# Kernel optimization log

Measured on AMD Instinct MI355X. Metric: run time of the kernel, lower is better.

Reference implementation:

```python
import jax, jax.numpy as jnp
import numpy as np

NUM_KNNS = 200
TEMPERATURE = 0.07
NUM_CLASSES = 1000


def setup_inputs() -> dict:
    key = jax.random.key(0)
    k1, k2, k3, k4 = jax.random.split(key, 4)
    N, D, K = 1024, 512, 65536
    # features and queue are L2-normalized (queue init is normal_l2)
    features = jax.random.normal(k1, (N, D), jnp.float32)
    features = features / jnp.linalg.norm(features, axis=-1, keepdims=True)
    queue_features = jax.random.normal(k2, (K, D), jnp.float32)
    queue_features = queue_features / jnp.linalg.norm(queue_features, axis=-1, keepdims=True)
    labels = jax.random.randint(k3, (N,), 0, NUM_CLASSES, dtype=jnp.int32)
    queue_labels = jax.random.randint(k4, (K,), 0, NUM_CLASSES, dtype=jnp.int32)
    return {
        "features": features,
        "queue_features": queue_features,
        "labels": labels,
        "queue_labels": queue_labels,
        "queue_ptr": 0,
    }


def reference(features, queue_features, labels, queue_labels, queue_ptr):
    # --- kNN accuracy ---
    # similarity matmul: [N, K]
    sim = jnp.einsum('nd,kd->nk', features, queue_features)
    sim_weight, sim_indices = jax.lax.top_k(sim, k=NUM_KNNS)  # [N, k]
    sim_weight = jnp.exp(sim_weight / TEMPERATURE)
    # gather neighbor labels (equivalent to the one-hot einsum in the original)
    sim_labels = queue_labels[sim_indices]  # [N, k] int32
    one_hot_labels = jax.nn.one_hot(sim_labels, NUM_CLASSES, dtype=sim_weight.dtype)  # [N, k, C]
    pred_scores = jnp.sum(one_hot_labels * sim_weight[..., None], axis=1)  # [N, C]
    pred_labels = jnp.argmax(pred_scores, axis=-1)
    accuracy = jnp.mean((pred_labels == labels).astype(jnp.float32))

    # --- circular queue scatter update ---
    N = features.shape[0]
    K = queue_features.shape[0]
    inds = jnp.arange(N) + queue_ptr
    new_queue_features = queue_features.at[inds].set(features)
    new_queue_labels = queue_labels.at[inds].set(labels)
    new_queue_ptr = (queue_ptr + N) % K
    return accuracy, new_queue_features, new_queue_labels, new_queue_ptr
```

## Files before the change

### kernel.cpp

```cpp
#include <hip/hip_runtime.h>
#include <math.h>

#define N_ROWS 1024
#define DIM    512
#define KQ     65536
#define KNN    200
#define NCLS   1000
#define NBINS  4096
#define CAP    2048
#define INV_T  14.285714285714286f

typedef unsigned short u16;
typedef __attribute__((ext_vector_type(8))) short short8;
typedef __attribute__((ext_vector_type(4))) float f32x4;
struct alignas(8) U16x4 { u16 x, y, z, w; };

#define GLOAD_LDS16(g, l)                                               \
    __builtin_amdgcn_global_load_lds(                                   \
        (__attribute__((address_space(1))) void*)(g),                   \
        (__attribute__((address_space(3))) void*)(l), 16, 0, 0)

__device__ __forceinline__ void split1(float x, u16& h, u16& l) {
    unsigned u = __float_as_uint(x);
    unsigned hr = (u + 0x7FFFu + ((u >> 16) & 1u)) >> 16;
    float hf = __uint_as_float(hr << 16);
    float lo = x - hf;
    unsigned ul = __float_as_uint(lo);
    unsigned lr = (ul + 0x7FFFu + ((ul >> 16) & 1u)) >> 16;
    h = (u16)hr; l = (u16)lr;
}

#define QF_BLOCKS (KQ * DIM / 4 / 256)
#define FT_BLOCKS (N_ROWS * DIM / 4 / 256)

__global__ __launch_bounds__(256) void fused_update_split_kernel(
    const float* __restrict__ feats, const float* __restrict__ qf,
    const int* __restrict__ labels, const int* __restrict__ ql,
    const int* __restrict__ qptr,
    float* __restrict__ out_qf, float* __restrict__ out_ql,
    float* __restrict__ out_ptr,
    u16* __restrict__ Bhi, u16* __restrict__ Blo,
    u16* __restrict__ Ahi, u16* __restrict__ Alo) {
    int ptr = qptr[0];
    int b = blockIdx.x;
    if (b < QF_BLOCKS) {
        size_t t = (size_t)b * 256 + threadIdx.x;
        size_t idx = t * 4;
        int row = (int)(idx >> 9);
        int col = (int)(idx & 511);
        float4 v = *(const float4*)(qf + idx);
        U16x4 h, l;
        split1(v.x, h.x, l.x); split1(v.y, h.y, l.y);
        split1(v.z, h.z, l.z); split1(v.w, h.w, l.w);
        *(U16x4*)(Bhi + idx) = h;
        *(U16x4*)(Blo + idx) = l;
        int d = row - ptr; if (d < 0) d += KQ;
        float4 o = (d < N_ROWS) ? *(const float4*)(feats + (size_t)d * DIM + col) : v;
        *(float4*)(out_qf + idx) = o;
        if (col == 0)
            out_ql[row] = (float)((d < N_ROWS) ? labels[d] : ql[row]);
    } else {
        size_t t = (size_t)(b - QF_BLOCKS) * 256 + threadIdx.x;
        size_t idx = t * 4;
        float4 v = *(const float4*)(feats + idx);
        U16x4 h, l;
        split1(v.x, h.x, l.x); split1(v.y, h.y, l.y);
        split1(v.z, h.z, l.z); split1(v.w, h.w, l.w);
        *(U16x4*)(Ahi + idx) = h;
        *(U16x4*)(Alo + idx) = l;
        if (t == 0) out_ptr[0] = (float)((ptr + N_ROWS) % KQ);
    }
}

#define NKT 24

#define STAGE8(kt_, dA, dB)                                                    \
  {                                                                            \
    const u16* Ap_ = ((kt_) < 16) ? Ahi : Alo;                                 \
    const u16* Bp_ = (((kt_) >> 3) == 1) ? Blo : Bhi;                          \
    int ke_ = ((kt_) & 7) << 6;                                                \
    const u16* ga_ = Ap_ + (size_t)(r0A + srow) * DIM + ke_ + scol;            \
    const u16* gb_ = Bp_ + (size_t)(r0B + srow) * DIM + ke_ + scol;            \
    GLOAD_LDS16(ga_ + (size_t)(8 * w0) * DIM,         &dA[0][w0 * 512]);       \
    GLOAD_LDS16(ga_ + (size_t)(8 * w1) * DIM,         &dA[0][w1 * 512]);       \
    GLOAD_LDS16(ga_ + (size_t)(128 + 8 * w0) * DIM,   &dA[1][w0 * 512]);       \
    GLOAD_LDS16(ga_ + (size_t)(128 + 8 * w1) * DIM,   &dA[1][w1 * 512]);       \
    GLOAD_LDS16(gb_ + (size_t)(8 * w0) * DIM,         &dB[0][w0 * 512]);       \
    GLOAD_LDS16(gb_ + (size_t)(8 * w1) * DIM,         &dB[0][w1 * 512]);       \
    GLOAD_LDS16(gb_ + (size_t)(128 + 8 * w0) * DIM,   &dB[1][w0 * 512]);       \
    GLOAD_LDS16(gb_ + (size_t)(128 + 8 * w1) * DIM,   &dB[1][w1 * 512]);       \
  }

#define MM(t_, u_)                                                             \
  acc[t_][u_] = __builtin_amdgcn_mfma_f32_16x16x32_bf16(                       \
      fa[(t_) & 3][0], fb[u_][0], acc[t_][u_], 0, 0, 0);                       \
  acc[t_][u_] = __builtin_amdgcn_mfma_f32_16x16x32_bf16(                       \
      fa[(t_) & 3][1], fb[u_][1], acc[t_][u_], 0, 0, 0);

#define TILE(kt_, RA, RB, SA, SB, DO_STAGE)                                    \
  {                                                                            \
    asm volatile("s_waitcnt vmcnt(0)" ::: "memory");                           \
    __builtin_amdgcn_s_barrier();                                              \
    const u16* aH_ = &RA[wm][0];                                               \
    const u16* bH_ = &RB[wn >> 1][bB];                                         \
                                                                  \
    _Pragma("unroll") for (int t = 0; t < 4; ++t) {                            \
      fa[t][0] = *(const short8*)(aH_ + t * 1024 + aoff + c0);                 \
      fa[t][1] = *(const short8*)(aH_ + t * 1024 + aoff + c1);                 \
    }                                                                          \
    _Pragma("unroll") for (int u = 0; u < 2; ++u) {                            \
      fb[u][0] = *(const short8*)(bH_ + u * 1024 + aoff + c0);                 \
      fb[u][1] = *(const short8*)(bH_ + u * 1024 + aoff + c1);                 \
    }                                                                          \
    if (DO_STAGE) STAGE8((kt_) + 1, SA, SB);                                   \
    __builtin_amdgcn_s_barrier();                                              \
    __builtin_amdgcn_s_setprio(1);                                             \
    _Pragma("unroll") for (int t = 0; t < 4; ++t) {                            \
      MM(t, 0); MM(t, 1);                                                      \
    }                                                                          \
    __builtin_amdgcn_s_setprio(0);                                             \
    __builtin_amdgcn_s_barrier();                                              \
                                                                  \
    _Pragma("unroll") for (int u = 2; u < 4; ++u) {                            \
      fb[u][0] = *(const short8*)(bH_ + u * 1024 + aoff + c0);                 \
      fb[u][1] = *(const short8*)(bH_ + u * 1024 + aoff + c1);                 \
    }                                                                          \
    __builtin_amdgcn_s_barrier();                                              \
    __builtin_amdgcn_s_setprio(1);                                             \
    _Pragma("unroll") for (int t = 0; t < 4; ++t) {                            \
      MM(t, 2); MM(t, 3);                                                      \
    }                                                                          \
    __builtin_amdgcn_s_setprio(0);                                             \
    __builtin_amdgcn_s_barrier();                                              \
                                                                  \
    _Pragma("unroll") for (int t = 0; t < 4; ++t) {                            \
      fa[t][0] = *(const short8*)(aH_ + (t + 4) * 1024 + aoff + c0);           \
      fa[t][1] = *(const short8*)(aH_ + (t + 4) * 1024 + aoff + c1);           \
    }                                                                          \
    __builtin_amdgcn_s_barrier();                                              \
    __builtin_amdgcn_s_setprio(1);                                             \
    _Pragma("unroll") for (int t = 4; t < 8; ++t) {                            \
      MM(t, 2); MM(t, 3);                                                      \
    }                                                                          \
    __builtin_amdgcn_s_setprio(0);                                             \
    __builtin_amdgcn_s_barrier();                                              \
                                                                  \
    __builtin_amdgcn_s_setprio(1);                                             \
    _Pragma("unroll") for (int t = 4; t < 8; ++t) {                            \
      MM(t, 0); MM(t, 1);                                                      \
    }                                                                          \
    __builtin_amdgcn_s_setprio(0);                                             \
  }

__global__ __launch_bounds__(512, 2) void gemm256_kernel(
    const u16* __restrict__ Ahi, const u16* __restrict__ Alo,
    const u16* __restrict__ Bhi, const u16* __restrict__ Blo,
    float* __restrict__ C) {
    __shared__ u16 sA0[2][8192], sB0[2][8192];
    __shared__ u16 sA1[2][8192], sB1[2][8192];

    int tid = threadIdx.x;
    int wv = tid >> 6, lane = tid & 63;
    int r = lane & 15, q = lane >> 4;
    int wm = wv >> 2, wn = wv & 3;
    int srow = lane >> 3;
    int scol = ((lane & 7) ^ (lane >> 3)) << 3;
    int w0 = wv, w1 = wv + 8;
    int aoff = r << 6;
    int c0 = (q << 3) ^ ((r & 7) << 3);
    int c1 = (32 | (q << 3)) ^ ((r & 7) << 3);
    int bB = (wn & 1) << 12;
    int r0A = blockIdx.y << 8;
    int r0B = blockIdx.x << 8;

    f32x4 acc[8][4] = {};
    short8 fa[4][2], fb[4][2];

    STAGE8(0, sA0, sB0);

    for (int kt = 0; kt < NKT; kt += 2) {
        TILE(kt,     sA0, sB0, sA1, sB1, 1);
        TILE(kt + 1, sA1, sB1, sA0, sB0, (kt + 2) < NKT);
    }

#pragma unroll
    for (int t = 0; t < 8; ++t)
#pragma unroll
        for (int u = 0; u < 4; ++u)
#pragma unroll
            for (int g = 0; g < 4; ++g) {
                int row = r0A + wm * 128 + t * 16 + q * 4 + g;
                int col = r0B + wn * 64 + u * 16 + r;
                C[(size_t)row * KQ + col] = acc[t][u][g];
            }
}

__global__ __launch_bounds__(256, 4) void gemm_mfma_kernel(
    const u16* __restrict__ Ahi, const u16* __restrict__ Alo,
    const u16* __restrict__ Bhi, const u16* __restrict__ Blo,
    float* __restrict__ C) {
    __shared__ u16 sA[2][128 * 32];
    __shared__ u16 sB[2][128 * 32];

    int tid = threadIdx.x;
    int wave = tid >> 6, lane = tid & 63;
    int q = lane >> 4, r = lane & 15;
    int bn = blockIdx.x, bm = blockIdx.y;
    int wm = wave & 1, wn = wave >> 1;

    const u16* gplane = (wave == 0) ? Ahi : (wave == 1) ? Alo
                      : (wave == 2) ? Bhi : Blo;
    int prow0 = (wave < 2) ? bm * 128 : bn * 128;
    const u16* gbase = gplane + (size_t)prow0 * DIM;
    u16* lbase = (wave == 0) ? sA[0] : (wave == 1) ? sA[1]
               : (wave == 2) ? sB[0] : sB[1];
    int lrow = lane >> 2;
    int lchunk = lane & 3;

    f32x4 acc[4][4] = {};

    for (int kt = 0; kt < DIM; kt += 32) {
        __syncthreads();
#pragma unroll
        for (int s = 0; s < 8; ++s) {
            const u16* g = gbase + (size_t)(s * 16 + lrow) * DIM + kt + lchunk * 8;
            GLOAD_LDS16(g, lbase + s * 512);
        }
        __syncthreads();

        short8 fa[2][4], fb[2][4];
#pragma unroll
        for (int t = 0; t < 4; ++t) {
            int am = wm * 64 + t * 16 + r;
            fa[0][t] = *(const short8*)&sA[0][am * 32 + q * 8];
            fa[1][t] = *(const short8*)&sA[1][am * 32 + q * 8];
            int bn_ = wn * 64 + t * 16 + r;
            fb[0][t] = *(const short8*)&sB[0][bn_ * 32 + q * 8];
            fb[1][t] = *(const short8*)&sB[1][bn_ * 32 + q * 8];
        }
#pragma unroll
        for (int i = 0; i < 4; ++i)
#pragma unroll
            for (int j = 0; j < 4; ++j) {
                acc[i][j] = __builtin_amdgcn_mfma_f32_16x16x32_bf16(
                    fa[0][i], fb[0][j], acc[i][j], 0, 0, 0);
                acc[i][j] = __builtin_amdgcn_mfma_f32_16x16x32_bf16(
                    fa[0][i], fb[1][j], acc[i][j], 0, 0, 0);
                acc[i][j] = __builtin_amdgcn_mfma_f32_16x16x32_bf16(
                    fa[1][i], fb[0][j], acc[i][j], 0, 0, 0);
            }
    }

#pragma unroll
    for (int i = 0; i < 4; ++i)
#pragma unroll
        for (int j = 0; j < 4; ++j)
#pragma unroll
            for (int g = 0; g < 4; ++g) {
                int row = bm * 128 + wm * 64 + i * 16 + q * 4 + g;
                int col = bn * 128 + wn * 64 + j * 16 + r;
                C[(size_t)row * KQ + col] = acc[i][j][g];
            }
}

#define LSTR 68
#define LA(k, m) ((k) * LSTR + (m))

__global__ __launch_bounds__(256) void gemm_nt_kernel(
    const float* __restrict__ A, const float* __restrict__ B,
    float* __restrict__ C) {
    __shared__ float As[32 * LSTR];
    __shared__ float Bs[32 * LSTR];
    int tid = threadIdx.x;
    int bn = blockIdx.x, bm = blockIdx.y;
    int tx = tid & 15, ty = tid >> 4;
    int lm = tid >> 3;
    int lk = (tid & 7) * 4;
    const float* Ab = A + (size_t)bm * 64 * DIM;
    const float* Bb = B + (size_t)bn * 64 * DIM;
    float acc[4][4] = {};
    for (int kt = 0; kt < DIM; kt += 32) {
        float4 a0 = *(const float4*)(Ab + (size_t)lm * DIM + kt + lk);
        float4 a1 = *(const float4*)(Ab + (size_t)(lm + 32) * DIM + kt + lk);
        float4 b0 = *(const float4*)(Bb + (size_t)lm * DIM + kt + lk);
        float4 b1 = *(const float4*)(Bb + (size_t)(lm + 32) * DIM + kt + lk);
        __syncthreads();
        As[LA(lk + 0, lm)] = a0.x;  As[LA(lk + 1, lm)] = a0.y;
        As[LA(lk + 2, lm)] = a0.z;  As[LA(lk + 3, lm)] = a0.w;
        As[LA(lk + 0, lm + 32)] = a1.x;  As[LA(lk + 1, lm + 32)] = a1.y;
        As[LA(lk + 2, lm + 32)] = a1.z;  As[LA(lk + 3, lm + 32)] = a1.w;
        Bs[LA(lk + 0, lm)] = b0.x;  Bs[LA(lk + 1, lm)] = b0.y;
        Bs[LA(lk + 2, lm)] = b0.z;  Bs[LA(lk + 3, lm)] = b0.w;
        Bs[LA(lk + 0, lm + 32)] = b1.x;  Bs[LA(lk + 1, lm + 32)] = b1.y;
        Bs[LA(lk + 2, lm + 32)] = b1.z;  Bs[LA(lk + 3, lm + 32)] = b1.w;
        __syncthreads();
#pragma unroll
        for (int kk = 0; kk < 32; ++kk) {
            float4 av = *(const float4*)&As[LA(kk, ty * 4)];
            float4 bv = *(const float4*)&Bs[LA(kk, tx * 4)];
            float a_[4] = {av.x, av.y, av.z, av.w};
            float b_[4] = {bv.x, bv.y, bv.z, bv.w};
#pragma unroll
            for (int i = 0; i < 4; ++i)
#pragma unroll
                for (int j = 0; j < 4; ++j) acc[i][j] += a_[i] * b_[j];
        }
    }
    for (int i = 0; i < 4; ++i) {
        float4 o = make_float4(acc[i][0], acc[i][1], acc[i][2], acc[i][3]);
        *(float4*)(C + (size_t)(bm * 64 + ty * 4 + i) * KQ + bn * 64 + tx * 4) = o;
    }
}

__device__ __forceinline__ unsigned order_key(float v) {
    unsigned u = __float_as_uint(v);
    return u ^ ((u & 0x80000000u) ? 0xFFFFFFFFu : 0x80000000u);
}

__global__ __launch_bounds__(1024) void topk_kernel(
    const float* __restrict__ sim, int r0,
    const int* __restrict__ ql, const int* __restrict__ labels,
    float* __restrict__ flags) {
    __shared__ unsigned hist[NBINS];
    __shared__ float cval[CAP];
    __shared__ int   cidx[CAP];
    __shared__ float scores[NCLS];
    __shared__ unsigned wsum[16];
    __shared__ float rb[16];
    __shared__ int   rc[16];
    __shared__ int s_bstar, s_ncand;

    int row = blockIdx.x;
    int tid = threadIdx.x;
    int lane = tid & 63;
    int wv = tid >> 6;
    const float4* s4 = (const float4*)(sim + (size_t)row * KQ);

    hist[tid] = 0; hist[tid + 1024] = 0; hist[tid + 2048] = 0; hist[tid + 3072] = 0;
    if (tid == 0) s_ncand = 0;
    __syncthreads();

    for (int i4 = tid; i4 < KQ / 4; i4 += 1024) {
        float4 v = s4[i4];
        atomicAdd(&hist[order_key(v.x) >> 20], 1u);
        atomicAdd(&hist[order_key(v.y) >> 20], 1u);
        atomicAdd(&hist[order_key(v.z) >> 20], 1u);
        atomicAdd(&hist[order_key(v.w) >> 20], 1u);
    }
    __syncthreads();

    unsigned loc = hist[4 * tid] + hist[4 * tid + 1] +
                   hist[4 * tid + 2] + hist[4 * tid + 3];
    unsigned x = loc;
#pragma unroll
    for (int off = 1; off < 64; off <<= 1) {
        unsigned y = __shfl_down(x, off);
        if (lane + off < 64) x += y;
    }
    if (lane == 0) wsum[wv] = x;
    __syncthreads();
    unsigned above = 0;
#pragma unroll
    for (int w2 = 0; w2 < 16; ++w2)
        if (w2 > wv) above += wsum[w2];
    unsigned running = above + x - loc;
    for (int j = 3; j >= 0; --j) {
        unsigned c = hist[4 * tid + j];
        if (running < KNN && running + c >= KNN) s_bstar = 4 * tid + j;
        running += c;
    }
    __syncthreads();
    int bstar = s_bstar;

    for (int i4 = tid; i4 < KQ / 4; i4 += 1024) {
        float4 v = s4[i4];
        float vv[4] = {v.x, v.y, v.z, v.w};
#pragma unroll
        for (int c = 0; c < 4; ++c) {
            if ((int)(order_key(vv[c]) >> 20) >= bstar) {
                int p = atomicAdd(&s_ncand, 1);
                if (p < CAP) { cval[p] = vv[c]; cidx[p] = i4 * 4 + c; }
            }
        }
    }
    if (tid < NCLS) scores[tid] = 0.f;
    __syncthreads();

    int M = s_ncand; if (M > CAP) M = CAP;
    for (int c = tid; c < M; c += 1024) {
        float v = cval[c]; int id = cidx[c];
        int rank = 0;
        for (int j = 0; j < M; ++j) {
            float vj = cval[j];
            if (vj > v || (vj == v && cidx[j] < id)) rank++;
        }
        if (rank < KNN) {
            float w = expf(v * INV_T);
            atomicAdd(&scores[ql[id]], w);
        }
    }
    __syncthreads();

    float b2 = (tid < NCLS) ? scores[tid] : -1.f;
    int   c2 = (tid < NCLS) ? tid : 0x3FFFFFFF;
#pragma unroll
    for (int off = 1; off < 64; off <<= 1) {
        float ob = __shfl_down(b2, off);
        int   oc = __shfl_down(c2, off);
        if (lane + off < 64 && (ob > b2 || (ob == b2 && oc < c2))) { b2 = ob; c2 = oc; }
    }
    if (lane == 0) { rb[wv] = b2; rc[wv] = c2; }
    __syncthreads();
    if (tid < 64) {
        float b3 = -1.f; int c3 = 0x3FFFFFFF;
        if (tid < 16) { b3 = rb[tid]; c3 = rc[tid]; }
#pragma unroll
        for (int off = 1; off < 16; off <<= 1) {
            float ob = __shfl_down(b3, off);
            int   oc = __shfl_down(c3, off);
            if (tid + off < 16 && (ob > b3 || (ob == b3 && oc < c3))) { b3 = ob; c3 = oc; }
        }
        if (tid == 0)
            flags[r0 + row] = (c3 == labels[r0 + row]) ? 1.0f : 0.0f;
    }
}

__global__ __launch_bounds__(256) void acc_kernel(
    const float* __restrict__ flags, float* __restrict__ out) {
    __shared__ float r[256];
    int tid = threadIdx.x;
    r[tid] = flags[tid] + flags[tid + 256] + flags[tid + 512] + flags[tid + 768];
    __syncthreads();
    for (int off = 128; off; off >>= 1) {
        if (tid < off) r[tid] += r[tid + off];
        __syncthreads();
    }
    if (tid == 0) out[0] = r[0] * (1.0f / 1024.0f);
}

extern "C" void kernel_launch(void* const* d_in, const int* in_sizes, int n_in,
                              void* d_out, int out_size, void* d_ws, size_t ws_size,
                              hipStream_t stream) {
    const float* feats  = (const float*)d_in[0];
    const float* qf     = (const float*)d_in[1];
    const int*   labels = (const int*)d_in[2];
    const int*   ql     = (const int*)d_in[3];
    const int*   qptr   = (const int*)d_in[4];

    float* out     = (float*)d_out;
    float* out_qf  = out + 1;
    float* out_ql  = out_qf + (size_t)KQ * DIM;
    float* out_ptr = out_ql + KQ;

    const size_t bplane = (size_t)KQ * DIM;
    const size_t aplane = (size_t)N_ROWS * DIM;

    int CH = 0;
    for (int c = 512; c >= 128; c >>= 1) {
        size_t need = 2 * bplane * 2 + 2 * aplane * 2 +
                      (size_t)c * KQ * 4 + N_ROWS * 4;
        if (need <= ws_size) { CH = c; break; }
    }

    if (CH > 0) {
        u16* Bhi = (u16*)d_ws;
        u16* Blo = Bhi + bplane;
        u16* Ahi = Blo + bplane;
        u16* Alo = Ahi + aplane;
        float* sim   = (float*)(Alo + aplane);
        float* flags = sim + (size_t)CH * KQ;

        fused_update_split_kernel<<<QF_BLOCKS + FT_BLOCKS, 256, 0, stream>>>(
            feats, qf, labels, ql, qptr, out_qf, out_ql, out_ptr,
            Bhi, Blo, Ahi, Alo);

        int nchunks = N_ROWS / CH;
        for (int c = 0; c < nchunks; ++c) {
            if (CH >= 256) {
                dim3 g(KQ / 256, CH / 256);
                gemm256_kernel<<<g, 512, 0, stream>>>(
                    Ahi + (size_t)c * CH * DIM, Alo + (size_t)c * CH * DIM,
                    Bhi, Blo, sim);
            } else {
                dim3 g(KQ / 128, CH / 128);
                gemm_mfma_kernel<<<g, 256, 0, stream>>>(
                    Ahi + (size_t)c * CH * DIM, Alo + (size_t)c * CH * DIM,
                    Bhi, Blo, sim);
            }
            topk_kernel<<<CH, 1024, 0, stream>>>(sim, c * CH, ql, labels, flags);
        }
        acc_kernel<<<1, 256, 0, stream>>>(flags, out);
    } else {
        int CHf = 256;
        while (CHf > 64 &&
               ((size_t)CHf * KQ * sizeof(float) + N_ROWS * sizeof(float)) > ws_size)
            CHf >>= 1;
        float* sim   = (float*)d_ws;
        float* flags = (float*)((char*)d_ws + (size_t)CHf * KQ * sizeof(float));
        fused_update_split_kernel<<<QF_BLOCKS + FT_BLOCKS, 256, 0, stream>>>(
            feats, qf, labels, ql, qptr, out_qf, out_ql, out_ptr,
            (u16*)sim, (u16*)sim, (u16*)sim, (u16*)sim);
        int nchunks = N_ROWS / CHf;
        for (int c = 0; c < nchunks; ++c) {
            const float* A = feats + (size_t)c * CHf * DIM;
            dim3 g(KQ / 64, CHf / 64);
            gemm_nt_kernel<<<g, 256, 0, stream>>>(A, qf, sim);
            topk_kernel<<<CHf, 1024, 0, stream>>>(sim, c * CHf, ql, labels, flags);
        }
        acc_kernel<<<1, 256, 0, stream>>>(flags, out);
    }
}
```

Before: 579.6 us.

## Use per-wave-pair packed 16-bit histograms and 512-thread blocks in top-k

The top-k kernel now runs with 512 threads per block and builds four privatized histograms, one per pair of waves. Each histogram has 2048 bins packed as two 16-bit counters per 32-bit word. This is meant to reduce LDS atomic contention during histogramming and to shrink the block for better occupancy. The coarser bins (shift by 21 instead of 20) can admit more candidates past the threshold, which raises the O(M^2) rank cost and the risk of overflowing CAP.

```diff
diff --git a/kernel.cpp b/kernel.cpp
--- a/kernel.cpp
+++ b/kernel.cpp
@@ -6,7 +6,6 @@
 #define KQ     65536
 #define KNN    200
 #define NCLS   1000
-#define NBINS  4096
 #define CAP    2048
 #define INV_T  14.285714285714286f
 
@@ -312,22 +311,25 @@
     }
 }
 
+#define NB2   2048
+#define NW2   1024
+
 __device__ __forceinline__ unsigned order_key(float v) {
     unsigned u = __float_as_uint(v);
     return u ^ ((u & 0x80000000u) ? 0xFFFFFFFFu : 0x80000000u);
 }
 
-__global__ __launch_bounds__(1024) void topk_kernel(
+__global__ __launch_bounds__(512) void topk_kernel(
     const float* __restrict__ sim, int r0,
     const int* __restrict__ ql, const int* __restrict__ labels,
     float* __restrict__ flags) {
-    __shared__ unsigned hist[NBINS];
+    __shared__ unsigned wh[4][NW2];
     __shared__ float cval[CAP];
     __shared__ int   cidx[CAP];
     __shared__ float scores[NCLS];
-    __shared__ unsigned wsum[16];
-    __shared__ float rb[16];
-    __shared__ int   rc[16];
+    __shared__ unsigned wsum[8];
+    __shared__ float rb[8];
+    __shared__ int   rc[8];
     __shared__ int s_bstar, s_ncand;
 
     int row = blockIdx.x;
@@ -336,21 +338,33 @@
     int wv = tid >> 6;
     const float4* s4 = (const float4*)(sim + (size_t)row * KQ);
 
-    hist[tid] = 0; hist[tid + 1024] = 0; hist[tid + 2048] = 0; hist[tid + 3072] = 0;
+#pragma unroll
+    for (int i = 0; i < 8; ++i) ((unsigned*)wh)[tid + 512 * i] = 0;
     if (tid == 0) s_ncand = 0;
     __syncthreads();
 
-    for (int i4 = tid; i4 < KQ / 4; i4 += 1024) {
+    unsigned* myh = wh[wv >> 1];
+    for (int i4 = tid; i4 < KQ / 4; i4 += 512) {
         float4 v = s4[i4];
-        atomicAdd(&hist[order_key(v.x) >> 20], 1u);
-        atomicAdd(&hist[order_key(v.y) >> 20], 1u);
-        atomicAdd(&hist[order_key(v.z) >> 20], 1u);
-        atomicAdd(&hist[order_key(v.w) >> 20], 1u);
-    }
-    __syncthreads();
-
-    unsigned loc = hist[4 * tid] + hist[4 * tid + 1] +
-                   hist[4 * tid + 2] + hist[4 * tid + 3];
+        unsigned k0 = order_key(v.x) >> 21, k1 = order_key(v.y) >> 21;
+        unsigned k2 = order_key(v.z) >> 21, k3 = order_key(v.w) >> 21;
+        atomicAdd(&myh[k0 >> 1], 1u << ((k0 & 1) << 4));
+        atomicAdd(&myh[k1 >> 1], 1u << ((k1 & 1) << 4));
+        atomicAdd(&myh[k2 >> 1], 1u << ((k2 & 1) << 4));
+        atomicAdd(&myh[k3 >> 1], 1u << ((k3 & 1) << 4));
+    }
+    __syncthreads();
+
+    unsigned cnt0 = 0, cnt1 = 0, cnt2 = 0, cnt3 = 0;
+#pragma unroll
+    for (int c = 0; c < 4; ++c) {
+        unsigned a = wh[c][2 * tid];
+        unsigned b = wh[c][2 * tid + 1];
+        cnt0 += a & 0xFFFFu; cnt1 += a >> 16;
+        cnt2 += b & 0xFFFFu; cnt3 += b >> 16;
+    }
+    unsigned loc = cnt0 + cnt1 + cnt2 + cnt3;
+
     unsigned x = loc;
 #pragma unroll
     for (int off = 1; off < 64; off <<= 1) {
@@ -361,33 +375,36 @@
     __syncthreads();
     unsigned above = 0;
 #pragma unroll
-    for (int w2 = 0; w2 < 16; ++w2)
+    for (int w2 = 0; w2 < 8; ++w2)
         if (w2 > wv) above += wsum[w2];
     unsigned running = above + x - loc;
+    unsigned cnts[4] = {cnt0, cnt1, cnt2, cnt3};
+#pragma unroll
     for (int j = 3; j >= 0; --j) {
-        unsigned c = hist[4 * tid + j];
+        unsigned c = cnts[j];
         if (running < KNN && running + c >= KNN) s_bstar = 4 * tid + j;
         running += c;
     }
     __syncthreads();
     int bstar = s_bstar;
 
-    for (int i4 = tid; i4 < KQ / 4; i4 += 1024) {
+    for (int i4 = tid; i4 < KQ / 4; i4 += 512) {
         float4 v = s4[i4];
         float vv[4] = {v.x, v.y, v.z, v.w};
 #pragma unroll
         for (int c = 0; c < 4; ++c) {
-            if ((int)(order_key(vv[c]) >> 20) >= bstar) {
+            if ((int)(order_key(vv[c]) >> 21) >= bstar) {
                 int p = atomicAdd(&s_ncand, 1);
                 if (p < CAP) { cval[p] = vv[c]; cidx[p] = i4 * 4 + c; }
             }
         }
     }
-    if (tid < NCLS) scores[tid] = 0.f;
+    scores[tid] = 0.f;
+    if (tid + 512 < NCLS) scores[tid + 512] = 0.f;
     __syncthreads();
 
     int M = s_ncand; if (M > CAP) M = CAP;
-    for (int c = tid; c < M; c += 1024) {
+    for (int c = tid; c < M; c += 512) {
         float v = cval[c]; int id = cidx[c];
         int rank = 0;
         for (int j = 0; j < M; ++j) {
@@ -401,8 +418,10 @@
     }
     __syncthreads();
 
-    float b2 = (tid < NCLS) ? scores[tid] : -1.f;
-    int   c2 = (tid < NCLS) ? tid : 0x3FFFFFFF;
+    float sa = (tid < NCLS) ? scores[tid] : -1.f;
+    float sb = (tid + 512 < NCLS) ? scores[tid + 512] : -1.f;
+    float b2; int c2;
+    if (sb > sa) { b2 = sb; c2 = tid + 512; } else { b2 = sa; c2 = tid; }
 #pragma unroll
     for (int off = 1; off < 64; off <<= 1) {
         float ob = __shfl_down(b2, off);
@@ -413,12 +432,12 @@
     __syncthreads();
     if (tid < 64) {
         float b3 = -1.f; int c3 = 0x3FFFFFFF;
-        if (tid < 16) { b3 = rb[tid]; c3 = rc[tid]; }
-#pragma unroll
-        for (int off = 1; off < 16; off <<= 1) {
+        if (tid < 8) { b3 = rb[tid]; c3 = rc[tid]; }
+#pragma unroll
+        for (int off = 1; off < 8; off <<= 1) {
             float ob = __shfl_down(b3, off);
             int   oc = __shfl_down(c3, off);
-            if (tid + off < 16 && (ob > b3 || (ob == b3 && oc < c3))) { b3 = ob; c3 = oc; }
+            if (tid + off < 8 && (ob > b3 || (ob == b3 && oc < c3))) { b3 = ob; c3 = oc; }
         }
         if (tid == 0)
             flags[r0 + row] = (c3 == labels[r0 + row]) ? 1.0f : 0.0f;
@@ -487,7 +506,7 @@
                     Ahi + (size_t)c * CH * DIM, Alo + (size_t)c * CH * DIM,
                     Bhi, Blo, sim);
             }
-            topk_kernel<<<CH, 1024, 0, stream>>>(sim, c * CH, ql, labels, flags);
+            topk_kernel<<<CH, 512, 0, stream>>>(sim, c * CH, ql, labels, flags);
         }
         acc_kernel<<<1, 256, 0, stream>>>(flags, out);
     } else {
@@ -505,7 +524,7 @@
             const float* A = feats + (size_t)c * CHf * DIM;
             dim3 g(KQ / 64, CHf / 64);
             gemm_nt_kernel<<<g, 256, 0, stream>>>(A, qf, sim);
-            topk_kernel<<<CHf, 1024, 0, stream>>>(sim, c * CHf, ql, labels, flags);
+            topk_kernel<<<CHf, 512, 0, stream>>>(sim, c * CHf, ql, labels, flags);
         }
         acc_kernel<<<1, 256, 0, stream>>>(flags, out);
     }
```

New measurement: 629.1 us. 8.5% more time.

## Emit 16-bit order keys from GEMM epilogue and scan keys in top-k

Applied to the files above, without the earlier changes.

The GEMM epilogue now writes a 16-bit monotone order key for every similarity next to the fp32 value. The top-k kernel builds its histogram and selects candidates by reading these half-width keys, then gathers the full fp32 values only for the candidates. This is meant to halve the bytes read in the two full-row passes of top-k. In exchange the GEMM writes an extra 2 bytes per element with scattered 16-bit stores, and the workspace grows, which may shrink the chunk size.

```diff
diff --git a/kernel.cpp b/kernel.cpp
--- a/kernel.cpp
+++ b/kernel.cpp
@@ -19,6 +19,11 @@
     __builtin_amdgcn_global_load_lds(                                   \
         (__attribute__((address_space(1))) void*)(g),                   \
         (__attribute__((address_space(3))) void*)(l), 16, 0, 0)
+
+__device__ __forceinline__ unsigned order_key(float v) {
+    unsigned u = __float_as_uint(v);
+    return u ^ ((u & 0x80000000u) ? 0xFFFFFFFFu : 0x80000000u);
+}
 
 __device__ __forceinline__ void split1(float x, u16& h, u16& l) {
     unsigned u = __float_as_uint(x);
@@ -155,7 +160,7 @@
 __global__ __launch_bounds__(512, 2) void gemm256_kernel(
     const u16* __restrict__ Ahi, const u16* __restrict__ Alo,
     const u16* __restrict__ Bhi, const u16* __restrict__ Blo,
-    float* __restrict__ C) {
+    float* __restrict__ C, u16* __restrict__ Ck) {
     __shared__ u16 sA0[2][8192], sB0[2][8192];
     __shared__ u16 sA1[2][8192], sB1[2][8192];
 
@@ -191,14 +196,17 @@
             for (int g = 0; g < 4; ++g) {
                 int row = r0A + wm * 128 + t * 16 + q * 4 + g;
                 int col = r0B + wn * 64 + u * 16 + r;
-                C[(size_t)row * KQ + col] = acc[t][u][g];
+                float v = acc[t][u][g];
+                size_t off = (size_t)row * KQ + col;
+                C[off] = v;
+                Ck[off] = (u16)(order_key(v) >> 16);
             }
 }
 
 __global__ __launch_bounds__(256, 4) void gemm_mfma_kernel(
     const u16* __restrict__ Ahi, const u16* __restrict__ Alo,
     const u16* __restrict__ Bhi, const u16* __restrict__ Blo,
-    float* __restrict__ C) {
+    float* __restrict__ C, u16* __restrict__ Ck) {
     __shared__ u16 sA[2][128 * 32];
     __shared__ u16 sB[2][128 * 32];
 
@@ -259,7 +267,10 @@
             for (int g = 0; g < 4; ++g) {
                 int row = bm * 128 + wm * 64 + i * 16 + q * 4 + g;
                 int col = bn * 128 + wn * 64 + j * 16 + r;
-                C[(size_t)row * KQ + col] = acc[i][j][g];
+                float v = acc[i][j][g];
+                size_t off = (size_t)row * KQ + col;
+                C[off] = v;
+                Ck[off] = (u16)(order_key(v) >> 16);
             }
 }
 
@@ -312,13 +323,20 @@
     }
 }
 
-__device__ __forceinline__ unsigned order_key(float v) {
-    unsigned u = __float_as_uint(v);
-    return u ^ ((u & 0x80000000u) ? 0xFFFFFFFFu : 0x80000000u);
+__global__ __launch_bounds__(256) void keygen_kernel(
+    const float* __restrict__ sim, u16* __restrict__ keys) {
+    size_t i = ((size_t)blockIdx.x * 256 + threadIdx.x) * 4;
+    float4 v = *(const float4*)(sim + i);
+    U16x4 k;
+    k.x = (u16)(order_key(v.x) >> 16);
+    k.y = (u16)(order_key(v.y) >> 16);
+    k.z = (u16)(order_key(v.z) >> 16);
+    k.w = (u16)(order_key(v.w) >> 16);
+    *(U16x4*)(keys + i) = k;
 }
 
 __global__ __launch_bounds__(1024) void topk_kernel(
-    const float* __restrict__ sim, int r0,
+    const float* __restrict__ sim, const u16* __restrict__ keys, int r0,
     const int* __restrict__ ql, const int* __restrict__ labels,
     float* __restrict__ flags) {
     __shared__ unsigned hist[NBINS];
@@ -334,18 +352,23 @@
     int tid = threadIdx.x;
     int lane = tid & 63;
     int wv = tid >> 6;
-    const float4* s4 = (const float4*)(sim + (size_t)row * KQ);
+    const uint4* k8 = (const uint4*)(keys + (size_t)row * KQ);
+    const float* srow = sim + (size_t)row * KQ;
 
     hist[tid] = 0; hist[tid + 1024] = 0; hist[tid + 2048] = 0; hist[tid + 3072] = 0;
     if (tid == 0) s_ncand = 0;
     __syncthreads();
 
-    for (int i4 = tid; i4 < KQ / 4; i4 += 1024) {
-        float4 v = s4[i4];
-        atomicAdd(&hist[order_key(v.x) >> 20], 1u);
-        atomicAdd(&hist[order_key(v.y) >> 20], 1u);
-        atomicAdd(&hist[order_key(v.z) >> 20], 1u);
-        atomicAdd(&hist[order_key(v.w) >> 20], 1u);
+    for (int i8 = tid; i8 < KQ / 8; i8 += 1024) {
+        uint4 w = k8[i8];
+        atomicAdd(&hist[(w.x >> 4) & 0xFFFu], 1u);
+        atomicAdd(&hist[ w.x >> 20          ], 1u);
+        atomicAdd(&hist[(w.y >> 4) & 0xFFFu], 1u);
+        atomicAdd(&hist[ w.y >> 20          ], 1u);
+        atomicAdd(&hist[(w.z >> 4) & 0xFFFu], 1u);
+        atomicAdd(&hist[ w.z >> 20          ], 1u);
+        atomicAdd(&hist[(w.w >> 4) & 0xFFFu], 1u);
+        atomicAdd(&hist[ w.w >> 20          ], 1u);
     }
     __syncthreads();
 
@@ -372,21 +395,29 @@
     __syncthreads();
     int bstar = s_bstar;
 
-    for (int i4 = tid; i4 < KQ / 4; i4 += 1024) {
-        float4 v = s4[i4];
-        float vv[4] = {v.x, v.y, v.z, v.w};
-#pragma unroll
-        for (int c = 0; c < 4; ++c) {
-            if ((int)(order_key(vv[c]) >> 20) >= bstar) {
+    for (int i8 = tid; i8 < KQ / 8; i8 += 1024) {
+        uint4 w = k8[i8];
+        int base = i8 * 8;
+        unsigned words[4] = {w.x, w.y, w.z, w.w};
+#pragma unroll
+        for (int t = 0; t < 4; ++t) {
+            if ((int)((words[t] >> 4) & 0xFFFu) >= bstar) {
                 int p = atomicAdd(&s_ncand, 1);
-                if (p < CAP) { cval[p] = vv[c]; cidx[p] = i4 * 4 + c; }
+                if (p < CAP) cidx[p] = base + 2 * t;
             }
+            if ((int)(words[t] >> 20) >= bstar) {
+                int p = atomicAdd(&s_ncand, 1);
+                if (p < CAP) cidx[p] = base + 2 * t + 1;
+            }
         }
     }
     if (tid < NCLS) scores[tid] = 0.f;
     __syncthreads();
 
     int M = s_ncand; if (M > CAP) M = CAP;
+    for (int c = tid; c < M; c += 1024) cval[c] = srow[cidx[c]];
+    __syncthreads();
+
     for (int c = tid; c < M; c += 1024) {
         float v = cval[c]; int id = cidx[c];
         int rank = 0;
@@ -458,7 +489,7 @@
     int CH = 0;
     for (int c = 512; c >= 128; c >>= 1) {
         size_t need = 2 * bplane * 2 + 2 * aplane * 2 +
-                      (size_t)c * KQ * 4 + N_ROWS * 4;
+                      (size_t)c * KQ * 4 + (size_t)c * KQ * 2 + N_ROWS * 4;
         if (need <= ws_size) { CH = c; break; }
     }
 
@@ -468,7 +499,8 @@
         u16* Ahi = Blo + bplane;
         u16* Alo = Ahi + aplane;
         float* sim   = (float*)(Alo + aplane);
-        float* flags = sim + (size_t)CH * KQ;
+        u16*   keys  = (u16*)(sim + (size_t)CH * KQ);
+        float* flags = (float*)(keys + (size_t)CH * KQ);
 
         fused_update_split_kernel<<<QF_BLOCKS + FT_BLOCKS, 256, 0, stream>>>(
             feats, qf, labels, ql, qptr, out_qf, out_ql, out_ptr,
@@ -480,23 +512,24 @@
                 dim3 g(KQ / 256, CH / 256);
                 gemm256_kernel<<<g, 512, 0, stream>>>(
                     Ahi + (size_t)c * CH * DIM, Alo + (size_t)c * CH * DIM,
-                    Bhi, Blo, sim);
+                    Bhi, Blo, sim, keys);
             } else {
                 dim3 g(KQ / 128, CH / 128);
                 gemm_mfma_kernel<<<g, 256, 0, stream>>>(
                     Ahi + (size_t)c * CH * DIM, Alo + (size_t)c * CH * DIM,
-                    Bhi, Blo, sim);
+                    Bhi, Blo, sim, keys);
             }
-            topk_kernel<<<CH, 1024, 0, stream>>>(sim, c * CH, ql, labels, flags);
+            topk_kernel<<<CH, 1024, 0, stream>>>(sim, keys, c * CH, ql, labels, flags);
         }
         acc_kernel<<<1, 256, 0, stream>>>(flags, out);
     } else {
         int CHf = 256;
         while (CHf > 64 &&
-               ((size_t)CHf * KQ * sizeof(float) + N_ROWS * sizeof(float)) > ws_size)
+               ((size_t)CHf * KQ * 6 + N_ROWS * sizeof(float)) > ws_size)
             CHf >>= 1;
         float* sim   = (float*)d_ws;
-        float* flags = (float*)((char*)d_ws + (size_t)CHf * KQ * sizeof(float));
+        u16*   keys  = (u16*)(sim + (size_t)CHf * KQ);
+        float* flags = (float*)(keys + (size_t)CHf * KQ);
         fused_update_split_kernel<<<QF_BLOCKS + FT_BLOCKS, 256, 0, stream>>>(
             feats, qf, labels, ql, qptr, out_qf, out_ql, out_ptr,
             (u16*)sim, (u16*)sim, (u16*)sim, (u16*)sim);
@@ -505,7 +538,9 @@
             const float* A = feats + (size_t)c * CHf * DIM;
             dim3 g(KQ / 64, CHf / 64);
             gemm_nt_kernel<<<g, 256, 0, stream>>>(A, qf, sim);
-            topk_kernel<<<CHf, 1024, 0, stream>>>(sim, c * CHf, ql, labels, flags);
+            keygen_kernel<<<(int)((size_t)CHf * KQ / 4 / 256), 256, 0, stream>>>(
+                sim, keys);
+            topk_kernel<<<CHf, 1024, 0, stream>>>(sim, keys, c * CHf, ql, labels, flags);
         }
         acc_kernel<<<1, 256, 0, stream>>>(flags, out);
     }
```

Result: no change. 578.0 us (-0.3%).

## Collect top-k candidates above a threshold in the GEMM epilogue

Applied to the files above, without the earlier changes.

The GEMM epilogues now compare each similarity against a fixed threshold and append qualifying values and column indices to per-row candidate buffers through global atomic counters. The top-k kernel then reads only these candidates when the count lies between KNN and the capacity, skipping the two full-row histogram and filter passes over 65536 similarities. The histogram path stays as a fallback. The cost is global atomics and scattered writes in the epilogue. The threshold is tuned to the cosine-similarity distribution of random unit vectors, so the fast path depends on the input statistics, while the fallback keeps results correct.

```diff
diff --git a/kernel.cpp b/kernel.cpp
--- a/kernel.cpp
+++ b/kernel.cpp
@@ -8,7 +8,9 @@
 #define NCLS   1000
 #define NBINS  4096
 #define CAP    2048
+#define CAPG   1536
 #define INV_T  14.285714285714286f
+#define THRESH 0.10f
 
 typedef unsigned short u16;
 typedef __attribute__((ext_vector_type(8))) short short8;
@@ -19,6 +21,11 @@
     __builtin_amdgcn_global_load_lds(                                   \
         (__attribute__((address_space(1))) void*)(g),                   \
         (__attribute__((address_space(3))) void*)(l), 16, 0, 0)
+
+__device__ __forceinline__ unsigned order_key(float v) {
+    unsigned u = __float_as_uint(v);
+    return u ^ ((u & 0x80000000u) ? 0xFFFFFFFFu : 0x80000000u);
+}
 
 __device__ __forceinline__ void split1(float x, u16& h, u16& l) {
     unsigned u = __float_as_uint(x);
@@ -40,7 +47,8 @@
     float* __restrict__ out_qf, float* __restrict__ out_ql,
     float* __restrict__ out_ptr,
     u16* __restrict__ Bhi, u16* __restrict__ Blo,
-    u16* __restrict__ Ahi, u16* __restrict__ Alo) {
+    u16* __restrict__ Ahi, u16* __restrict__ Alo,
+    int* __restrict__ cnt) {
     int ptr = qptr[0];
     int b = blockIdx.x;
     if (b < QF_BLOCKS) {
@@ -68,6 +76,7 @@
         split1(v.z, h.z, l.z); split1(v.w, h.w, l.w);
         *(U16x4*)(Ahi + idx) = h;
         *(U16x4*)(Alo + idx) = l;
+        if (t < N_ROWS / 4) ((int4*)cnt)[t] = make_int4(0, 0, 0, 0);
         if (t == 0) out_ptr[0] = (float)((ptr + N_ROWS) % KQ);
     }
 }
@@ -155,7 +164,8 @@
 __global__ __launch_bounds__(512, 2) void gemm256_kernel(
     const u16* __restrict__ Ahi, const u16* __restrict__ Alo,
     const u16* __restrict__ Bhi, const u16* __restrict__ Blo,
-    float* __restrict__ C) {
+    float* __restrict__ C, int* __restrict__ cnt,
+    float* __restrict__ candv, int* __restrict__ candi) {
     __shared__ u16 sA0[2][8192], sB0[2][8192];
     __shared__ u16 sA1[2][8192], sB1[2][8192];
 
@@ -191,14 +201,23 @@
             for (int g = 0; g < 4; ++g) {
                 int row = r0A + wm * 128 + t * 16 + q * 4 + g;
                 int col = r0B + wn * 64 + u * 16 + r;
-                C[(size_t)row * KQ + col] = acc[t][u][g];
+                float v = acc[t][u][g];
+                C[(size_t)row * KQ + col] = v;
+                if (v > THRESH) {
+                    int p = atomicAdd(&cnt[row], 1);
+                    if (p < CAPG) {
+                        candv[(size_t)row * CAPG + p] = v;
+                        candi[(size_t)row * CAPG + p] = col;
+                    }
+                }
             }
 }
 
 __global__ __launch_bounds__(256, 4) void gemm_mfma_kernel(
     const u16* __restrict__ Ahi, const u16* __restrict__ Alo,
     const u16* __restrict__ Bhi, const u16* __restrict__ Blo,
-    float* __restrict__ C) {
+    float* __restrict__ C, int* __restrict__ cnt,
+    float* __restrict__ candv, int* __restrict__ candi) {
     __shared__ u16 sA[2][128 * 32];
     __shared__ u16 sB[2][128 * 32];
 
@@ -259,7 +278,15 @@
             for (int g = 0; g < 4; ++g) {
                 int row = bm * 128 + wm * 64 + i * 16 + q * 4 + g;
                 int col = bn * 128 + wn * 64 + j * 16 + r;
-                C[(size_t)row * KQ + col] = acc[i][j][g];
+                float v = acc[i][j][g];
+                C[(size_t)row * KQ + col] = v;
+                if (v > THRESH) {
+                    int p = atomicAdd(&cnt[row], 1);
+                    if (p < CAPG) {
+                        candv[(size_t)row * CAPG + p] = v;
+                        candi[(size_t)row * CAPG + p] = col;
+                    }
+                }
             }
 }
 
@@ -312,13 +339,9 @@
     }
 }
 
-__device__ __forceinline__ unsigned order_key(float v) {
-    unsigned u = __float_as_uint(v);
-    return u ^ ((u & 0x80000000u) ? 0xFFFFFFFFu : 0x80000000u);
-}
-
 __global__ __launch_bounds__(1024) void topk_kernel(
-    const float* __restrict__ sim, int r0,
+    const float* __restrict__ sim, const int* __restrict__ cnt,
+    const float* __restrict__ candv, const int* __restrict__ candi, int r0,
     const int* __restrict__ ql, const int* __restrict__ labels,
     float* __restrict__ flags) {
     __shared__ unsigned hist[NBINS];
@@ -336,57 +359,68 @@
     int wv = tid >> 6;
     const float4* s4 = (const float4*)(sim + (size_t)row * KQ);
 
-    hist[tid] = 0; hist[tid + 1024] = 0; hist[tid + 2048] = 0; hist[tid + 3072] = 0;
-    if (tid == 0) s_ncand = 0;
-    __syncthreads();
-
-    for (int i4 = tid; i4 < KQ / 4; i4 += 1024) {
-        float4 v = s4[i4];
-        atomicAdd(&hist[order_key(v.x) >> 20], 1u);
-        atomicAdd(&hist[order_key(v.y) >> 20], 1u);
-        atomicAdd(&hist[order_key(v.z) >> 20], 1u);
-        atomicAdd(&hist[order_key(v.w) >> 20], 1u);
-    }
-    __syncthreads();
-
-    unsigned loc = hist[4 * tid] + hist[4 * tid + 1] +
-                   hist[4 * tid + 2] + hist[4 * tid + 3];
-    unsigned x = loc;
-#pragma unroll
-    for (int off = 1; off < 64; off <<= 1) {
-        unsigned y = __shfl_down(x, off);
-        if (lane + off < 64) x += y;
-    }
-    if (lane == 0) wsum[wv] = x;
-    __syncthreads();
-    unsigned above = 0;
-#pragma unroll
-    for (int w2 = 0; w2 < 16; ++w2)
-        if (w2 > wv) above += wsum[w2];
-    unsigned running = above + x - loc;
-    for (int j = 3; j >= 0; --j) {
-        unsigned c = hist[4 * tid + j];
-        if (running < KNN && running + c >= KNN) s_bstar = 4 * tid + j;
-        running += c;
-    }
-    __syncthreads();
-    int bstar = s_bstar;
-
-    for (int i4 = tid; i4 < KQ / 4; i4 += 1024) {
-        float4 v = s4[i4];
-        float vv[4] = {v.x, v.y, v.z, v.w};
-#pragma unroll
-        for (int c = 0; c < 4; ++c) {
-            if ((int)(order_key(vv[c]) >> 20) >= bstar) {
-                int p = atomicAdd(&s_ncand, 1);
-                if (p < CAP) { cval[p] = vv[c]; cidx[p] = i4 * 4 + c; }
+    int M = cnt[row];
+    if (M >= KNN && M <= CAPG) {
+        for (int c = tid; c < M; c += 1024) {
+            cval[c] = candv[(size_t)row * CAPG + c];
+            cidx[c] = candi[(size_t)row * CAPG + c];
+        }
+    } else {
+        hist[tid] = 0; hist[tid + 1024] = 0;
+        hist[tid + 2048] = 0; hist[tid + 3072] = 0;
+        if (tid == 0) s_ncand = 0;
+        __syncthreads();
+
+        for (int i4 = tid; i4 < KQ / 4; i4 += 1024) {
+            float4 v = s4[i4];
+            atomicAdd(&hist[order_key(v.x) >> 20], 1u);
+            atomicAdd(&hist[order_key(v.y) >> 20], 1u);
+            atomicAdd(&hist[order_key(v.z) >> 20], 1u);
+            atomicAdd(&hist[order_key(v.w) >> 20], 1u);
+        }
+        __syncthreads();
+
+        unsigned loc = hist[4 * tid] + hist[4 * tid + 1] +
+                       hist[4 * tid + 2] + hist[4 * tid + 3];
+        unsigned x = loc;
+#pragma unroll
+        for (int off = 1; off < 64; off <<= 1) {
+            unsigned y = __shfl_down(x, off);
+            if (lane + off < 64) x += y;
+        }
+        if (lane == 0) wsum[wv] = x;
+        __syncthreads();
+        unsigned above = 0;
+#pragma unroll
+        for (int w2 = 0; w2 < 16; ++w2)
+            if (w2 > wv) above += wsum[w2];
+        unsigned running = above + x - loc;
+        for (int j = 3; j >= 0; --j) {
+            unsigned c = hist[4 * tid + j];
+            if (running < KNN && running + c >= KNN) s_bstar = 4 * tid + j;
+            running += c;
+        }
+        __syncthreads();
+        int bstar = s_bstar;
+
+        for (int i4 = tid; i4 < KQ / 4; i4 += 1024) {
+            float4 v = s4[i4];
+            float vv[4] = {v.x, v.y, v.z, v.w};
+#pragma unroll
+            for (int c = 0; c < 4; ++c) {
+                if ((int)(order_key(vv[c]) >> 20) >= bstar) {
+                    int p = atomicAdd(&s_ncand, 1);
+                    if (p < CAP) { cval[p] = vv[c]; cidx[p] = i4 * 4 + c; }
+                }
             }
         }
-    }
+        __syncthreads();
+        M = s_ncand; if (M > CAP) M = CAP;
+    }
+
     if (tid < NCLS) scores[tid] = 0.f;
     __syncthreads();
 
-    int M = s_ncand; if (M > CAP) M = CAP;
     for (int c = tid; c < M; c += 1024) {
         float v = cval[c]; int id = cidx[c];
         int rank = 0;
@@ -438,6 +472,10 @@
     if (tid == 0) out[0] = r[0] * (1.0f / 1024.0f);
 }
 
+__global__ __launch_bounds__(256) void zero_cnt_kernel(int* __restrict__ cnt) {
+    ((int4*)cnt)[threadIdx.x] = make_int4(0, 0, 0, 0);
+}
+
 extern "C" void kernel_launch(void* const* d_in, const int* in_sizes, int n_in,
                               void* d_out, int out_size, void* d_ws, size_t ws_size,
                               hipStream_t stream) {
@@ -454,11 +492,12 @@
 
     const size_t bplane = (size_t)KQ * DIM;
     const size_t aplane = (size_t)N_ROWS * DIM;
+    const size_t candsz = (size_t)N_ROWS * CAPG;
 
     int CH = 0;
     for (int c = 512; c >= 128; c >>= 1) {
         size_t need = 2 * bplane * 2 + 2 * aplane * 2 +
-                      (size_t)c * KQ * 4 + N_ROWS * 4;
+                      (size_t)c * KQ * 4 + candsz * 8 + N_ROWS * 4 + N_ROWS * 4;
         if (need <= ws_size) { CH = c; break; }
     }
 
@@ -467,45 +506,56 @@
         u16* Blo = Bhi + bplane;
         u16* Ahi = Blo + bplane;
         u16* Alo = Ahi + aplane;
-        float* sim   = (float*)(Alo + aplane);
-        float* flags = sim + (size_t)CH * KQ;
+        float* sim      = (float*)(Alo + aplane);
+        float* cand_val = sim + (size_t)CH * KQ;
+        int*   cand_idx = (int*)(cand_val + candsz);
+        int*   cnt      = (int*)(cand_idx + candsz);
+        float* flags    = (float*)(cnt + N_ROWS);
 
         fused_update_split_kernel<<<QF_BLOCKS + FT_BLOCKS, 256, 0, stream>>>(
             feats, qf, labels, ql, qptr, out_qf, out_ql, out_ptr,
-            Bhi, Blo, Ahi, Alo);
+            Bhi, Blo, Ahi, Alo, cnt);
 
         int nchunks = N_ROWS / CH;
         for (int c = 0; c < nchunks; ++c) {
+            int*   cnt_c = cnt + c * CH;
+            float* cv_c  = cand_val + (size_t)c * CH * CAPG;
+            int*   ci_c  = cand_idx + (size_t)c * CH * CAPG;
             if (CH >= 256) {
                 dim3 g(KQ / 256, CH / 256);
                 gemm256_kernel<<<g, 512, 0, stream>>>(
                     Ahi + (size_t)c * CH * DIM, Alo + (size_t)c * CH * DIM,
-                    Bhi, Blo, sim);
+                    Bhi, Blo, sim, cnt_c, cv_c, ci_c);
             } else {
                 dim3 g(KQ / 128, CH / 128);
                 gemm_mfma_kernel<<<g, 256, 0, stream>>>(
                     Ahi + (size_t)c * CH * DIM, Alo + (size_t)c * CH * DIM,
-                    Bhi, Blo, sim);
+                    Bhi, Blo, sim, cnt_c, cv_c, ci_c);
             }
-            topk_kernel<<<CH, 1024, 0, stream>>>(sim, c * CH, ql, labels, flags);
+            topk_kernel<<<CH, 1024, 0, stream>>>(
+                sim, cnt_c, cv_c, ci_c, c * CH, ql, labels, flags);
         }
         acc_kernel<<<1, 256, 0, stream>>>(flags, out);
     } else {
         int CHf = 256;
         while (CHf > 64 &&
-               ((size_t)CHf * KQ * sizeof(float) + N_ROWS * sizeof(float)) > ws_size)
+               ((size_t)CHf * KQ * sizeof(float) + N_ROWS * 8 + 4096) > ws_size)
             CHf >>= 1;
         float* sim   = (float*)d_ws;
-        float* flags = (float*)((char*)d_ws + (size_t)CHf * KQ * sizeof(float));
+        int*   cnt   = (int*)(sim + (size_t)CHf * KQ);
+        float* flags = (float*)(cnt + N_ROWS);
         fused_update_split_kernel<<<QF_BLOCKS + FT_BLOCKS, 256, 0, stream>>>(
             feats, qf, labels, ql, qptr, out_qf, out_ql, out_ptr,
-            (u16*)sim, (u16*)sim, (u16*)sim, (u16*)sim);
+            (u16*)sim, (u16*)sim, (u16*)sim, (u16*)sim, cnt);
+        zero_cnt_kernel<<<1, 256, 0, stream>>>(cnt);
         int nchunks = N_ROWS / CHf;
         for (int c = 0; c < nchunks; ++c) {
             const float* A = feats + (size_t)c * CHf * DIM;
             dim3 g(KQ / 64, CHf / 64);
             gemm_nt_kernel<<<g, 256, 0, stream>>>(A, qf, sim);
-            topk_kernel<<<CHf, 1024, 0, stream>>>(sim, c * CHf, ql, labels, flags);
+            topk_kernel<<<CHf, 1024, 0, stream>>>(
+                sim, cnt, (const float*)sim, (const int*)cnt, c * CHf,
+                ql, labels, flags);
         }
         acc_kernel<<<1, 256, 0, stream>>>(flags, out);
     }
```

New measurement: 1.965 ms. 3.39x slower.
